# Kernel tuning notes

Hardware: AMD Instinct MI355X
Metric: run time of the kernel (lower is better)

The kernel has to match this reference:

```python
import jax, jax.numpy as jnp
import numpy as np

N_NODES = 50000
N_EDGES = 800000
IN_CH = 64
OUT_CH = 64
N_REL = 8
N_BASES = 4
K_STEPS = 2


def setup_inputs() -> dict:
    key = jax.random.key(0)
    ks = jax.random.split(key, 7)
    x = jax.random.normal(ks[0], (N_NODES, IN_CH), dtype=jnp.float32)
    edge_index = jax.random.randint(ks[1], (2, N_EDGES), 0, N_NODES, dtype=jnp.int64)
    edge_attr = jax.random.uniform(ks[2], (N_EDGES, N_REL), dtype=jnp.float32)
    # stacked per-layer params (both layers are 64->64)
    scale = 1.0 / np.sqrt(IN_CH)
    basis = jax.random.normal(ks[3], (K_STEPS, N_BASES, IN_CH, OUT_CH), dtype=jnp.float32) * scale
    att = jax.random.normal(ks[4], (K_STEPS, N_REL, N_BASES), dtype=jnp.float32) * 0.5
    root = jax.random.normal(ks[5], (K_STEPS, IN_CH, OUT_CH), dtype=jnp.float32) * scale
    bias = jax.random.normal(ks[6], (K_STEPS, OUT_CH), dtype=jnp.float32) * 0.01
    return {"x": x, "edge_index": edge_index, "edge_attr": edge_attr,
            "basis": basis, "att": att, "root": root, "bias": bias}


def _rgcn_layer(h, src, dst, edge_attr, basis_k, att_k, root_k, bias_k):
    # w: [R, in, out] from basis decomposition
    w = jnp.einsum('rb,bio->rio', att_k, basis_k)
    # per-node per-relation transform [R, N, out] (N < E, cheaper than per-edge)
    xw = jnp.einsum('ni,rio->rno', h, w)
    # edge messages: sum_r edge_attr[e,r] * xw[r, src[e], :]
    msg = jnp.zeros((src.shape[0], xw.shape[-1]), dtype=h.dtype)
    for r in range(xw.shape[0]):  # fixed small relation count
        msg = msg + xw[r][src] * edge_attr[:, r][:, None]
    # scatter-add aggregation to target nodes
    agg = jax.ops.segment_sum(msg, dst, num_segments=h.shape[0])
    return agg + h @ root_k + bias_k


def reference(x, edge_index, edge_attr, basis, att, root, bias):
    src = edge_index[0]
    dst = edge_index[1]
    h = x
    for k in range(K_STEPS):
        h = _rgcn_layer(h, src, dst, edge_attr, basis[k], att[k], root[k], bias[k])
        if k != K_STEPS - 1:
            h = jax.nn.relu(h)
    return h
```

## Files before the change

kernel.cpp:

```cpp
#include <hip/hip_runtime.h>

#define N_NODES 50000
#define N_EDGES 800000
#define N_PADROWS 50048

typedef unsigned int uint;
typedef unsigned short ushort;

typedef __attribute__((ext_vector_type(8))) short short8;
typedef __attribute__((ext_vector_type(4))) float floatx4;

__device__ __forceinline__ ushort f2bf(float f) {
    uint u = __builtin_bit_cast(uint, f);
    u += 0x7fffu + ((u >> 16) & 1u);
    return (ushort)(u >> 16);
}
__device__ __forceinline__ float bf2f(ushort h) {
    uint u = ((uint)h) << 16;
    return __builtin_bit_cast(float, u);
}
__device__ __forceinline__ float bflo(uint w) { return __builtin_bit_cast(float, w << 16); }
__device__ __forceinline__ float bfhi(uint w) { return __builtin_bit_cast(float, w & 0xffff0000u); }
__device__ __forceinline__ uint pack2(float a, float b) {
    return (uint)f2bf(a) | ((uint)f2bf(b) << 16);
}

#define CONV_BLOCKS 1563
#define ZERO_BLOCKS 196
#define PREP_BLOCKS 160
#define INIT_BLOCKS (CONV_BLOCKS + ZERO_BLOCKS + PREP_BLOCKS)

__global__ __launch_bounds__(256) void init_k(const float* __restrict__ x,
                                              ushort* __restrict__ hb,
                                              int* __restrict__ counts,
                                              const float* __restrict__ basis,
                                              const float* __restrict__ root,
                                              ushort* __restrict__ Bsw) {
    int b = blockIdx.x;
    if (b < CONV_BLOCKS) {
        int i = b * 256 + threadIdx.x;
        if (i >= N_NODES * 8) return;
        const float4* p = (const float4*)(x + (size_t)i * 8);
        float4 a = p[0], c = p[1];
        uint4 o;
        o.x = pack2(a.x, a.y); o.y = pack2(a.z, a.w);
        o.z = pack2(c.x, c.y); o.w = pack2(c.z, c.w);
        *(uint4*)(hb + (size_t)i * 8) = o;
    } else if (b < CONV_BLOCKS + ZERO_BLOCKS) {
        int i = (b - CONV_BLOCKS) * 256 + threadIdx.x;
        if (i < N_NODES) counts[i] = 0;
    } else {
        int idx = (b - (CONV_BLOCKS + ZERO_BLOCKS)) * 256 + threadIdx.x;
        if (idx >= 2 * 20480) return;
        int l = idx / 20480;
        int r = idx % 20480;
        int kb = r >> 11, ct = (r >> 9) & 3, q = (r >> 7) & 3, n = (r >> 3) & 15, j = r & 7;
        int k = kb * 32 + q * 8 + j;
        int c = ct * 16 + n;
        float v = (k < 256) ? basis[(size_t)l * 16384 + k * 64 + c]
                            : root[(size_t)l * 4096 + (k - 256) * 64 + c];
        Bsw[idx] = f2bf(v);
    }
}


__global__ __launch_bounds__(256) void hist_k(const int* __restrict__ ei, int* __restrict__ counts) {
    int e = blockIdx.x * 256 + threadIdx.x;
    if (e < N_EDGES) atomicAdd(&counts[ei[N_EDGES + e]], 1);
}

__global__ __launch_bounds__(1024) void scan1_k(const int* __restrict__ counts,
                                                int* __restrict__ start,
                                                int* __restrict__ bsums) {
    __shared__ int s[1024];
    int i = blockIdx.x * 1024 + threadIdx.x;
    int x = (i < N_NODES) ? counts[i] : 0;
    s[threadIdx.x] = x;
    __syncthreads();
    for (int off = 1; off < 1024; off <<= 1) {
        int v = (threadIdx.x >= off) ? s[threadIdx.x - off] : 0;
        __syncthreads();
        s[threadIdx.x] += v;
        __syncthreads();
    }
    if (i < N_NODES) start[i] = s[threadIdx.x] - x;
    if (threadIdx.x == 1023) bsums[blockIdx.x] = s[1023];
}

__global__ void scan2_k(int* __restrict__ bsums, int nblocks) {
    int lane = threadIdx.x;
    int v = (lane < nblocks) ? bsums[lane] : 0;
    int x = v;
    #pragma unroll
    for (int off = 1; off < 64; off <<= 1) {
        int t = __shfl_up(x, off, 64);
        if (lane >= off) x += t;
    }
    if (lane < nblocks) bsums[lane] = x - v;
}

__global__ __launch_bounds__(256) void scan3_k(int* __restrict__ start,
                                               int* __restrict__ cursor,
                                               const int* __restrict__ bsums) {
    int i = blockIdx.x * 256 + threadIdx.x;
    if (i < N_NODES) {
        int v = start[i] + bsums[i >> 10];
        start[i] = v;
        cursor[i] = v;
    }
}

__global__ __launch_bounds__(256) void scatter_k(const int* __restrict__ ei,
                                                 const float* __restrict__ ea,
                                                 const float* __restrict__ att,
                                                 int* __restrict__ cursor,
                                                 uint4* __restrict__ rec) {
    int e = blockIdx.x * 256 + threadIdx.x;
    if (e >= N_EDGES) return;
    int src = ei[e];
    int dst = ei[N_EDGES + e];

    const float4* eav = (const float4*)(ea + (size_t)e * 8);
    float4 a0 = eav[0], a1 = eav[1];
    float ev[8] = {a0.x, a0.y, a0.z, a0.w, a1.x, a1.y, a1.z, a1.w};

    float4 c0 = make_float4(0.f, 0.f, 0.f, 0.f);
    float4 c1 = make_float4(0.f, 0.f, 0.f, 0.f);
    const float4* att0 = (const float4*)att;
    const float4* att1 = (const float4*)(att + 32);
    #pragma unroll
    for (int r = 0; r < 8; ++r) {
        float4 w0 = att0[r];
        float4 w1 = att1[r];
        c0.x = fmaf(ev[r], w0.x, c0.x); c0.y = fmaf(ev[r], w0.y, c0.y);
        c0.z = fmaf(ev[r], w0.z, c0.z); c0.w = fmaf(ev[r], w0.w, c0.w);
        c1.x = fmaf(ev[r], w1.x, c1.x); c1.y = fmaf(ev[r], w1.y, c1.y);
        c1.z = fmaf(ev[r], w1.z, c1.z); c1.w = fmaf(ev[r], w1.w, c1.w);
    }
    int pos = atomicAdd(&cursor[dst], 1);
    rec[2 * (size_t)pos]     = make_uint4((uint)src, pack2(c0.x, c0.y), pack2(c0.z, c0.w), 0u);
    rec[2 * (size_t)pos + 1] = make_uint4((uint)src, pack2(c1.x, c1.y), pack2(c1.z, c1.w), 0u);
}


__global__ __launch_bounds__(256) void agg_k(const int* __restrict__ start,
                                             const int* __restrict__ counts,
                                             const uint4* __restrict__ recs,
                                             const ushort* __restrict__ hb,
                                             ushort* __restrict__ y16) {
    int node = blockIdx.x * 4 + (threadIdx.x >> 6);
    int lane = threadIdx.x & 63;
    if (node >= N_NODES) return;
    int s = start[node];
    int cnt = counts[node];

    float y0 = 0.f, y1 = 0.f, y2 = 0.f, y3 = 0.f;
    int j = 0;
    for (; j + 7 < cnt; j += 8) {
        uint4 r[8];
        #pragma unroll
        for (int i = 0; i < 8; ++i) r[i] = recs[2 * (size_t)(s + j + i)];
        float hv[8];
        #pragma unroll
        for (int i = 0; i < 8; ++i) hv[i] = bf2f(hb[(size_t)r[i].x * 64 + lane]);
        #pragma unroll
        for (int i = 0; i < 8; ++i) {
            y0 = fmaf(bflo(r[i].y), hv[i], y0);
            y1 = fmaf(bfhi(r[i].y), hv[i], y1);
            y2 = fmaf(bflo(r[i].z), hv[i], y2);
            y3 = fmaf(bfhi(r[i].z), hv[i], y3);
        }
    }
    for (; j + 1 < cnt; j += 2) {
        uint4 ra = recs[2 * (size_t)(s + j)];
        uint4 rb = recs[2 * (size_t)(s + j + 1)];
        float ha = bf2f(hb[(size_t)ra.x * 64 + lane]);
        float hbv = bf2f(hb[(size_t)rb.x * 64 + lane]);
        y0 = fmaf(bflo(ra.y), ha, y0); y1 = fmaf(bfhi(ra.y), ha, y1);
        y2 = fmaf(bflo(ra.z), ha, y2); y3 = fmaf(bfhi(ra.z), ha, y3);
        y0 = fmaf(bflo(rb.y), hbv, y0); y1 = fmaf(bfhi(rb.y), hbv, y1);
        y2 = fmaf(bflo(rb.z), hbv, y2); y3 = fmaf(bfhi(rb.z), hbv, y3);
    }
    if (j < cnt) {
        uint4 r = recs[2 * (size_t)(s + j)];
        float hv = bf2f(hb[(size_t)r.x * 64 + lane]);
        y0 = fmaf(bflo(r.y), hv, y0); y1 = fmaf(bfhi(r.y), hv, y1);
        y2 = fmaf(bflo(r.z), hv, y2); y3 = fmaf(bfhi(r.z), hv, y3);
    }
    ushort* yr = y16 + (size_t)node * 256;
    yr[lane]       = f2bf(y0);
    yr[64 + lane]  = f2bf(y1);
    yr[128 + lane] = f2bf(y2);
    yr[192 + lane] = f2bf(y3);
}

__global__ __launch_bounds__(256) void gemm_k(const ushort* __restrict__ y16,
                                              const ushort* __restrict__ hb,
                                              const ushort* __restrict__ Bsw,
                                              const float* __restrict__ bias,
                                              float* __restrict__ outf,
                                              ushort* __restrict__ outh,
                                              int relu) {
    __shared__ uint4 bs[2560];
    const int tid = threadIdx.x;
    for (int i = tid; i < 2560; i += 256) bs[i] = ((const uint4*)Bsw)[i];

    const int lane = tid & 63;
    const int wid = tid >> 6;
    const int nlo = lane & 15;
    const int quad = lane >> 4;
    const int m0 = blockIdx.x * 64 + wid * 16;

    floatx4 acc[4];
    #pragma unroll
    for (int ct = 0; ct < 4; ++ct) acc[ct] = (floatx4){0.f, 0.f, 0.f, 0.f};

    const ushort* yrow = y16 + (size_t)(m0 + nlo) * 256 + quad * 8;
    const ushort* hrow = hb  + (size_t)(m0 + nlo) * 64  + quad * 8;
    __syncthreads();

    #pragma unroll
    for (int kb = 0; kb < 10; ++kb) {
        uint4 av = (kb < 8) ? *(const uint4*)(yrow + kb * 32)
                            : *(const uint4*)(hrow + (kb - 8) * 32);
        short8 a = __builtin_bit_cast(short8, av);
        #pragma unroll
        for (int ct = 0; ct < 4; ++ct) {
            short8 b = __builtin_bit_cast(short8, bs[(kb * 4 + ct) * 64 + lane]);
            acc[ct] = __builtin_amdgcn_mfma_f32_16x16x32_bf16(a, b, acc[ct], 0, 0, 0);
        }
    }

    #pragma unroll
    for (int ct = 0; ct < 4; ++ct) {
        int col = ct * 16 + nlo;
        float bv = bias[col];
        #pragma unroll
        for (int r = 0; r < 4; ++r) {
            int row = m0 + quad * 4 + r;
            if (row < N_NODES) {
                float v = acc[ct][r] + bv;
                if (relu) v = fmaxf(v, 0.f);
                if (outf) outf[(size_t)row * 64 + col] = v;
                if (outh) outh[(size_t)row * 64 + col] = f2bf(v);
            }
        }
    }
}


extern "C" void kernel_launch(void* const* d_in, const int* in_sizes, int n_in,
                              void* d_out, int out_size, void* d_ws, size_t ws_size,
                              hipStream_t stream) {
    const float* x     = (const float*)d_in[0];
    const int*   ei    = (const int*)d_in[1];
    const float* ea    = (const float*)d_in[2];
    const float* basis = (const float*)d_in[3];
    const float* att   = (const float*)d_in[4];
    const float* root  = (const float*)d_in[5];
    const float* bias  = (const float*)d_in[6];
    float* out = (float*)d_out;

    char* p = (char*)d_ws;
    uint4*  rec    = (uint4*)p;   p += (size_t)N_EDGES * 32;
    ushort* y16    = (ushort*)p;  p += (size_t)N_PADROWS * 256 * 2;
    ushort* hb0    = (ushort*)p;  p += (size_t)N_PADROWS * 64 * 2;
    ushort* hb1    = (ushort*)p;  p += (size_t)N_PADROWS * 64 * 2;
    ushort* Bsw    = (ushort*)p;  p += (size_t)2 * 20480 * 2;
    int*    counts = (int*)p;     p += (size_t)N_NODES * 4;
    int*    start  = (int*)p;     p += (size_t)N_NODES * 4;
    int*    cursor = (int*)p;     p += (size_t)N_NODES * 4;
    int*    bsums  = (int*)p;     p += 64 * 4;

    const int scan_blocks = (N_NODES + 1023) / 1024;

    init_k<<<INIT_BLOCKS, 256, 0, stream>>>(x, hb0, counts, basis, root, Bsw);
    hist_k<<<(N_EDGES + 255) / 256, 256, 0, stream>>>(ei, counts);
    scan1_k<<<scan_blocks, 1024, 0, stream>>>(counts, start, bsums);
    scan2_k<<<1, 64, 0, stream>>>(bsums, scan_blocks);
    scan3_k<<<(N_NODES + 255) / 256, 256, 0, stream>>>(start, cursor, bsums);
    scatter_k<<<(N_EDGES + 255) / 256, 256, 0, stream>>>(ei, ea, att, cursor, rec);

    dim3 agg_grid((N_NODES + 3) / 4);
    dim3 gemm_grid(N_PADROWS / 64);

    agg_k<<<agg_grid, 256, 0, stream>>>(start, counts, rec, hb0, y16);
    gemm_k<<<gemm_grid, 256, 0, stream>>>(y16, hb0, Bsw, bias, (float*)0, hb1, 1);

    agg_k<<<agg_grid, 256, 0, stream>>>(start, counts, rec + 1, hb1, y16);
    gemm_k<<<gemm_grid, 256, 0, stream>>>(y16, hb1, Bsw + 20480, bias + 64, out, (ushort*)0, 0);
}
```

Baseline: 272.5 us.

## Split CSR edge scatter into coarse bucket pass and local shared-memory pass

```diff
diff --git a/kernel.cpp b/kernel.cpp
--- a/kernel.cpp
+++ b/kernel.cpp
@@ -3,6 +3,7 @@
 #define N_NODES 50000
 #define N_EDGES 800000
 #define N_PADROWS 50048
+#define NB 782
 
 typedef unsigned int uint;
 typedef unsigned short ushort;
@@ -100,21 +101,21 @@
 }
 
 __global__ __launch_bounds__(256) void scan3_k(int* __restrict__ start,
-                                               int* __restrict__ cursor,
+                                               int* __restrict__ bcur,
                                                const int* __restrict__ bsums) {
     int i = blockIdx.x * 256 + threadIdx.x;
     if (i < N_NODES) {
         int v = start[i] + bsums[i >> 10];
         start[i] = v;
-        cursor[i] = v;
-    }
-}
-
-__global__ __launch_bounds__(256) void scatter_k(const int* __restrict__ ei,
-                                                 const float* __restrict__ ea,
-                                                 const float* __restrict__ att,
-                                                 int* __restrict__ cursor,
-                                                 uint4* __restrict__ rec) {
+        if ((i & 63) == 0) bcur[i >> 6] = v;
+    }
+}
+
+__global__ __launch_bounds__(256) void scatter1_k(const int* __restrict__ ei,
+                                                  const float* __restrict__ ea,
+                                                  const float* __restrict__ att,
+                                                  int* __restrict__ bcur,
+                                                  uint4* __restrict__ srec) {
     int e = blockIdx.x * 256 + threadIdx.x;
     if (e >= N_EDGES) return;
     int src = ei[e];
@@ -137,9 +138,31 @@
         c1.x = fmaf(ev[r], w1.x, c1.x); c1.y = fmaf(ev[r], w1.y, c1.y);
         c1.z = fmaf(ev[r], w1.z, c1.z); c1.w = fmaf(ev[r], w1.w, c1.w);
     }
-    int pos = atomicAdd(&cursor[dst], 1);
-    rec[2 * (size_t)pos]     = make_uint4((uint)src, pack2(c0.x, c0.y), pack2(c0.z, c0.w), 0u);
-    rec[2 * (size_t)pos + 1] = make_uint4((uint)src, pack2(c1.x, c1.y), pack2(c1.z, c1.w), 0u);
+    int pos = atomicAdd(&bcur[dst >> 6], 1);
+    srec[2 * (size_t)pos]     = make_uint4((uint)src, pack2(c0.x, c0.y), pack2(c0.z, c0.w), (uint)dst);
+    srec[2 * (size_t)pos + 1] = make_uint4((uint)src, pack2(c1.x, c1.y), pack2(c1.z, c1.w), 0u);
+}
+
+__global__ __launch_bounds__(256) void scatter2_k(const int* __restrict__ start,
+                                                  const uint4* __restrict__ srec,
+                                                  uint4* __restrict__ rec) {
+    __shared__ int lcur[64];
+    int b = blockIdx.x;
+    int n0 = b << 6;
+    if (threadIdx.x < 64) {
+        int n = n0 + threadIdx.x;
+        lcur[threadIdx.x] = (n < N_NODES) ? start[n] : N_EDGES;
+    }
+    int lo = start[n0];
+    int hi = (b == NB - 1) ? N_EDGES : start[n0 + 64];
+    __syncthreads();
+    for (int i = lo + threadIdx.x; i < hi; i += 256) {
+        uint4 r0 = srec[2 * (size_t)i];
+        uint4 r1 = srec[2 * (size_t)i + 1];
+        int slot = atomicAdd(&lcur[(int)r0.w - n0], 1);
+        rec[2 * (size_t)slot]     = r0;
+        rec[2 * (size_t)slot + 1] = r1;
+    }
 }
 
 
@@ -269,8 +292,10 @@
     ushort* Bsw    = (ushort*)p;  p += (size_t)2 * 20480 * 2;
     int*    counts = (int*)p;     p += (size_t)N_NODES * 4;
     int*    start  = (int*)p;     p += (size_t)N_NODES * 4;
-    int*    cursor = (int*)p;     p += (size_t)N_NODES * 4;
+    int*    bcur   = (int*)p;     p += (size_t)1024 * 4;
     int*    bsums  = (int*)p;     p += 64 * 4;
+
+    uint4* srec = (uint4*)y16;
 
     const int scan_blocks = (N_NODES + 1023) / 1024;
 
@@ -278,8 +303,9 @@
     hist_k<<<(N_EDGES + 255) / 256, 256, 0, stream>>>(ei, counts);
     scan1_k<<<scan_blocks, 1024, 0, stream>>>(counts, start, bsums);
     scan2_k<<<1, 64, 0, stream>>>(bsums, scan_blocks);
-    scan3_k<<<(N_NODES + 255) / 256, 256, 0, stream>>>(start, cursor, bsums);
-    scatter_k<<<(N_EDGES + 255) / 256, 256, 0, stream>>>(ei, ea, att, cursor, rec);
+    scan3_k<<<(N_NODES + 255) / 256, 256, 0, stream>>>(start, bcur, bsums);
+    scatter1_k<<<(N_EDGES + 255) / 256, 256, 0, stream>>>(ei, ea, att, bcur, srec);
+    scatter2_k<<<NB, 256, 0, stream>>>(start, srec, rec);
 
     dim3 agg_grid((N_NODES + 3) / 4);
     dim3 gemm_grid(N_PADROWS / 64);
```

Measured after the change: 438.1 us. 60.8% more time.

## Fuse neighbor aggregation with MFMA GEMM via LDS tile; batch two edges per scatter thread

Applied to the files above, without the earlier changes.

```diff
diff --git a/kernel.cpp b/kernel.cpp
--- a/kernel.cpp
+++ b/kernel.cpp
@@ -115,136 +115,135 @@
                                                  const float* __restrict__ att,
                                                  int* __restrict__ cursor,
                                                  uint4* __restrict__ rec) {
-    int e = blockIdx.x * 256 + threadIdx.x;
-    if (e >= N_EDGES) return;
-    int src = ei[e];
-    int dst = ei[N_EDGES + e];
-
-    const float4* eav = (const float4*)(ea + (size_t)e * 8);
-    float4 a0 = eav[0], a1 = eav[1];
-    float ev[8] = {a0.x, a0.y, a0.z, a0.w, a1.x, a1.y, a1.z, a1.w};
-
-    float4 c0 = make_float4(0.f, 0.f, 0.f, 0.f);
-    float4 c1 = make_float4(0.f, 0.f, 0.f, 0.f);
+    int e0 = blockIdx.x * 512 + threadIdx.x;
     const float4* att0 = (const float4*)att;
     const float4* att1 = (const float4*)(att + 32);
-    #pragma unroll
-    for (int r = 0; r < 8; ++r) {
-        float4 w0 = att0[r];
-        float4 w1 = att1[r];
-        c0.x = fmaf(ev[r], w0.x, c0.x); c0.y = fmaf(ev[r], w0.y, c0.y);
-        c0.z = fmaf(ev[r], w0.z, c0.z); c0.w = fmaf(ev[r], w0.w, c0.w);
-        c1.x = fmaf(ev[r], w1.x, c1.x); c1.y = fmaf(ev[r], w1.y, c1.y);
-        c1.z = fmaf(ev[r], w1.z, c1.z); c1.w = fmaf(ev[r], w1.w, c1.w);
-    }
-    int pos = atomicAdd(&cursor[dst], 1);
-    rec[2 * (size_t)pos]     = make_uint4((uint)src, pack2(c0.x, c0.y), pack2(c0.z, c0.w), 0u);
-    rec[2 * (size_t)pos + 1] = make_uint4((uint)src, pack2(c1.x, c1.y), pack2(c1.z, c1.w), 0u);
-}
-
-
-__global__ __launch_bounds__(256) void agg_k(const int* __restrict__ start,
-                                             const int* __restrict__ counts,
-                                             const uint4* __restrict__ recs,
-                                             const ushort* __restrict__ hb,
-                                             ushort* __restrict__ y16) {
-    int node = blockIdx.x * 4 + (threadIdx.x >> 6);
-    int lane = threadIdx.x & 63;
-    if (node >= N_NODES) return;
-    int s = start[node];
-    int cnt = counts[node];
-
-    float y0 = 0.f, y1 = 0.f, y2 = 0.f, y3 = 0.f;
-    int j = 0;
-    for (; j + 7 < cnt; j += 8) {
-        uint4 r[8];
+
+    int   src[2], dst[2];
+    float4 ca[2], cb[2];
+    bool  ok[2];
+
+    #pragma unroll
+    for (int u = 0; u < 2; ++u) {
+        int e = e0 + u * 256;
+        ok[u] = (e < N_EDGES);
+        if (!ok[u]) continue;
+        src[u] = ei[e];
+        dst[u] = ei[N_EDGES + e];
+        const float4* eav = (const float4*)(ea + (size_t)e * 8);
+        float4 a0 = eav[0], a1 = eav[1];
+        float ev[8] = {a0.x, a0.y, a0.z, a0.w, a1.x, a1.y, a1.z, a1.w};
+        float4 c0 = make_float4(0.f, 0.f, 0.f, 0.f);
+        float4 c1 = make_float4(0.f, 0.f, 0.f, 0.f);
         #pragma unroll
-        for (int i = 0; i < 8; ++i) r[i] = recs[2 * (size_t)(s + j + i)];
-        float hv[8];
-        #pragma unroll
-        for (int i = 0; i < 8; ++i) hv[i] = bf2f(hb[(size_t)r[i].x * 64 + lane]);
-        #pragma unroll
-        for (int i = 0; i < 8; ++i) {
-            y0 = fmaf(bflo(r[i].y), hv[i], y0);
-            y1 = fmaf(bfhi(r[i].y), hv[i], y1);
-            y2 = fmaf(bflo(r[i].z), hv[i], y2);
-            y3 = fmaf(bfhi(r[i].z), hv[i], y3);
-        }
-    }
-    for (; j + 1 < cnt; j += 2) {
-        uint4 ra = recs[2 * (size_t)(s + j)];
-        uint4 rb = recs[2 * (size_t)(s + j + 1)];
-        float ha = bf2f(hb[(size_t)ra.x * 64 + lane]);
-        float hbv = bf2f(hb[(size_t)rb.x * 64 + lane]);
-        y0 = fmaf(bflo(ra.y), ha, y0); y1 = fmaf(bfhi(ra.y), ha, y1);
-        y2 = fmaf(bflo(ra.z), ha, y2); y3 = fmaf(bfhi(ra.z), ha, y3);
-        y0 = fmaf(bflo(rb.y), hbv, y0); y1 = fmaf(bfhi(rb.y), hbv, y1);
-        y2 = fmaf(bflo(rb.z), hbv, y2); y3 = fmaf(bfhi(rb.z), hbv, y3);
-    }
-    if (j < cnt) {
-        uint4 r = recs[2 * (size_t)(s + j)];
-        float hv = bf2f(hb[(size_t)r.x * 64 + lane]);
-        y0 = fmaf(bflo(r.y), hv, y0); y1 = fmaf(bfhi(r.y), hv, y1);
-        y2 = fmaf(bflo(r.z), hv, y2); y3 = fmaf(bfhi(r.z), hv, y3);
-    }
-    ushort* yr = y16 + (size_t)node * 256;
-    yr[lane]       = f2bf(y0);
-    yr[64 + lane]  = f2bf(y1);
-    yr[128 + lane] = f2bf(y2);
-    yr[192 + lane] = f2bf(y3);
-}
-
-__global__ __launch_bounds__(256) void gemm_k(const ushort* __restrict__ y16,
-                                              const ushort* __restrict__ hb,
-                                              const ushort* __restrict__ Bsw,
-                                              const float* __restrict__ bias,
-                                              float* __restrict__ outf,
-                                              ushort* __restrict__ outh,
-                                              int relu) {
-    __shared__ uint4 bs[2560];
+        for (int r = 0; r < 8; ++r) {
+            float4 w0 = att0[r];
+            float4 w1 = att1[r];
+            c0.x = fmaf(ev[r], w0.x, c0.x); c0.y = fmaf(ev[r], w0.y, c0.y);
+            c0.z = fmaf(ev[r], w0.z, c0.z); c0.w = fmaf(ev[r], w0.w, c0.w);
+            c1.x = fmaf(ev[r], w1.x, c1.x); c1.y = fmaf(ev[r], w1.y, c1.y);
+            c1.z = fmaf(ev[r], w1.z, c1.z); c1.w = fmaf(ev[r], w1.w, c1.w);
+        }
+        ca[u] = c0; cb[u] = c1;
+    }
+
+    int pos[2];
+    #pragma unroll
+    for (int u = 0; u < 2; ++u)
+        if (ok[u]) pos[u] = atomicAdd(&cursor[dst[u]], 1);
+
+    #pragma unroll
+    for (int u = 0; u < 2; ++u) {
+        if (!ok[u]) continue;
+        rec[2 * (size_t)pos[u]]     = make_uint4((uint)src[u], pack2(ca[u].x, ca[u].y), pack2(ca[u].z, ca[u].w), 0u);
+        rec[2 * (size_t)pos[u] + 1] = make_uint4((uint)src[u], pack2(cb[u].x, cb[u].y), pack2(cb[u].z, cb[u].w), 0u);
+    }
+}
+
+__global__ __launch_bounds__(256) void aggemm_k(const int* __restrict__ start,
+                                                const int* __restrict__ counts,
+                                                const uint4* __restrict__ recs,
+                                                const ushort* __restrict__ hb,
+                                                const ushort* __restrict__ Bsw,
+                                                const float* __restrict__ bias,
+                                                float* __restrict__ outf,
+                                                ushort* __restrict__ outh,
+                                                int relu) {
+    __shared__ __align__(16) ushort ylds[16][264];
     const int tid = threadIdx.x;
-    for (int i = tid; i < 2560; i += 256) bs[i] = ((const uint4*)Bsw)[i];
-
     const int lane = tid & 63;
     const int wid = tid >> 6;
+    const int m0 = blockIdx.x * 16;
+
+    for (int t = 0; t < 4; ++t) {
+        int node = m0 + wid * 4 + t;
+        int s = start[node];
+        int cnt = counts[node];
+        float y0 = 0.f, y1 = 0.f, y2 = 0.f, y3 = 0.f;
+        int j = 0;
+        for (; j + 7 < cnt; j += 8) {
+            uint4 r[8];
+            #pragma unroll
+            for (int i = 0; i < 8; ++i) r[i] = recs[2 * (size_t)(s + j + i)];
+            float hv[8];
+            #pragma unroll
+            for (int i = 0; i < 8; ++i) hv[i] = bf2f(hb[(size_t)r[i].x * 64 + lane]);
+            #pragma unroll
+            for (int i = 0; i < 8; ++i) {
+                y0 = fmaf(bflo(r[i].y), hv[i], y0);
+                y1 = fmaf(bfhi(r[i].y), hv[i], y1);
+                y2 = fmaf(bflo(r[i].z), hv[i], y2);
+                y3 = fmaf(bfhi(r[i].z), hv[i], y3);
+            }
+        }
+        for (; j + 1 < cnt; j += 2) {
+            uint4 ra = recs[2 * (size_t)(s + j)];
+            uint4 rb = recs[2 * (size_t)(s + j + 1)];
+            float ha = bf2f(hb[(size_t)ra.x * 64 + lane]);
+            float hbv = bf2f(hb[(size_t)rb.x * 64 + lane]);
+            y0 = fmaf(bflo(ra.y), ha, y0); y1 = fmaf(bfhi(ra.y), ha, y1);
+            y2 = fmaf(bflo(ra.z), ha, y2); y3 = fmaf(bfhi(ra.z), ha, y3);
+            y0 = fmaf(bflo(rb.y), hbv, y0); y1 = fmaf(bfhi(rb.y), hbv, y1);
+            y2 = fmaf(bflo(rb.z), hbv, y2); y3 = fmaf(bfhi(rb.z), hbv, y3);
+        }
+        if (j < cnt) {
+            uint4 r = recs[2 * (size_t)(s + j)];
+            float hv = bf2f(hb[(size_t)r.x * 64 + lane]);
+            y0 = fmaf(bflo(r.y), hv, y0); y1 = fmaf(bfhi(r.y), hv, y1);
+            y2 = fmaf(bflo(r.z), hv, y2); y3 = fmaf(bfhi(r.z), hv, y3);
+        }
+        int nl = wid * 4 + t;
+        ylds[nl][lane]       = f2bf(y0);
+        ylds[nl][64 + lane]  = f2bf(y1);
+        ylds[nl][128 + lane] = f2bf(y2);
+        ylds[nl][192 + lane] = f2bf(y3);
+    }
+    __syncthreads();
+
     const int nlo = lane & 15;
     const int quad = lane >> 4;
-    const int m0 = blockIdx.x * 64 + wid * 16;
-
-    floatx4 acc[4];
-    #pragma unroll
-    for (int ct = 0; ct < 4; ++ct) acc[ct] = (floatx4){0.f, 0.f, 0.f, 0.f};
-
-    const ushort* yrow = y16 + (size_t)(m0 + nlo) * 256 + quad * 8;
-    const ushort* hrow = hb  + (size_t)(m0 + nlo) * 64  + quad * 8;
-    __syncthreads();
-
+    const int ct = wid;
+    floatx4 acc = (floatx4){0.f, 0.f, 0.f, 0.f};
+
+    const ushort* hrow = hb + (size_t)(m0 + nlo) * 64 + quad * 8;
     #pragma unroll
     for (int kb = 0; kb < 10; ++kb) {
-        uint4 av = (kb < 8) ? *(const uint4*)(yrow + kb * 32)
-                            : *(const uint4*)(hrow + (kb - 8) * 32);
-        short8 a = __builtin_bit_cast(short8, av);
-        #pragma unroll
-        for (int ct = 0; ct < 4; ++ct) {
-            short8 b = __builtin_bit_cast(short8, bs[(kb * 4 + ct) * 64 + lane]);
-            acc[ct] = __builtin_amdgcn_mfma_f32_16x16x32_bf16(a, b, acc[ct], 0, 0, 0);
-        }
-    }
-
-    #pragma unroll
-    for (int ct = 0; ct < 4; ++ct) {
-        int col = ct * 16 + nlo;
-        float bv = bias[col];
-        #pragma unroll
-        for (int r = 0; r < 4; ++r) {
-            int row = m0 + quad * 4 + r;
-            if (row < N_NODES) {
-                float v = acc[ct][r] + bv;
-                if (relu) v = fmaxf(v, 0.f);
-                if (outf) outf[(size_t)row * 64 + col] = v;
-                if (outh) outh[(size_t)row * 64 + col] = f2bf(v);
-            }
-        }
+        short8 a;
+        if (kb < 8) a = *(const short8*)&ylds[nlo][quad * 8 + kb * 32];
+        else        a = __builtin_bit_cast(short8, *(const uint4*)(hrow + (kb - 8) * 32));
+        short8 b = __builtin_bit_cast(short8, ((const uint4*)Bsw)[(kb * 4 + ct) * 64 + lane]);
+        acc = __builtin_amdgcn_mfma_f32_16x16x32_bf16(a, b, acc, 0, 0, 0);
+    }
+
+    int col = ct * 16 + nlo;
+    float bv = bias[col];
+    #pragma unroll
+    for (int r = 0; r < 4; ++r) {
+        int row = m0 + quad * 4 + r;
+        float v = acc[r] + bv;
+        if (relu) v = fmaxf(v, 0.f);
+        if (outf) outf[(size_t)row * 64 + col] = v;
+        if (outh) outh[(size_t)row * 64 + col] = f2bf(v);
     }
 }
 
@@ -263,7 +262,6 @@
 
     char* p = (char*)d_ws;
     uint4*  rec    = (uint4*)p;   p += (size_t)N_EDGES * 32;
-    ushort* y16    = (ushort*)p;  p += (size_t)N_PADROWS * 256 * 2;
     ushort* hb0    = (ushort*)p;  p += (size_t)N_PADROWS * 64 * 2;
     ushort* hb1    = (ushort*)p;  p += (size_t)N_PADROWS * 64 * 2;
     ushort* Bsw    = (ushort*)p;  p += (size_t)2 * 20480 * 2;
@@ -279,14 +277,11 @@
     scan1_k<<<scan_blocks, 1024, 0, stream>>>(counts, start, bsums);
     scan2_k<<<1, 64, 0, stream>>>(bsums, scan_blocks);
     scan3_k<<<(N_NODES + 255) / 256, 256, 0, stream>>>(start, cursor, bsums);
-    scatter_k<<<(N_EDGES + 255) / 256, 256, 0, stream>>>(ei, ea, att, cursor, rec);
-
-    dim3 agg_grid((N_NODES + 3) / 4);
-    dim3 gemm_grid(N_PADROWS / 64);
-
-    agg_k<<<agg_grid, 256, 0, stream>>>(start, counts, rec, hb0, y16);
-    gemm_k<<<gemm_grid, 256, 0, stream>>>(y16, hb0, Bsw, bias, (float*)0, hb1, 1);
-
-    agg_k<<<agg_grid, 256, 0, stream>>>(start, counts, rec + 1, hb1, y16);
-    gemm_k<<<gemm_grid, 256, 0, stream>>>(y16, hb1, Bsw + 20480, bias + 64, out, (ushort*)0, 0);
-}
+    scatter_k<<<(N_EDGES + 511) / 512, 256, 0, stream>>>(ei, ea, att, cursor, rec);
+
+    dim3 f_grid(N_NODES / 16);
+
+    aggemm_k<<<f_grid, 256, 0, stream>>>(start, counts, rec, hb0, Bsw, bias, (float*)0, hb1, 1);
+
+    aggemm_k<<<f_grid, 256, 0, stream>>>(start, counts, rec + 1, hb1, Bsw + 20480, bias + 64, out, (ushort*)0, 0);
+}
```

New measurement: 283.0 us. +3.8%, slower.
